# Kernel tuning notes

Hardware: AMD Instinct MI355X
Metric: run time of the kernel (lower is better)

The kernel has to match this reference:

```python
import jax, jax.numpy as jnp
import numpy as np

B, OUT, IN = 1024, 1024, 512


def setup_inputs() -> dict:
    key = jax.random.key(0)
    kx, kw = jax.random.split(key)
    X = jax.random.normal(kx, (B, IN), dtype=jnp.float32)
    # Xavier-uniform init for W [out_features, in_features]
    limit = float(np.sqrt(6.0 / (IN + OUT)))
    W = jax.random.uniform(kw, (OUT, IN), dtype=jnp.float32, minval=-limit, maxval=limit)
    return {"X": X, "W": W}


def reference(X, W):
    # tropical min-plus + max-plus 'matmul':
    # out[b,o] = min_i(W[o,i] + X[b,i]) + max_i(W[o,i] + X[b,i])
    S = X[:, None, :] + W[None, :, :]  # [B, OUT, IN]
    return jnp.min(S, axis=-1) + jnp.max(S, axis=-1)  # [B, OUT]
```

## Files before the change

### kernel.cpp

```cpp
#include <hip/hip_runtime.h>
#include <math.h>


typedef float f4 __attribute__((ext_vector_type(4)));

constexpr int B_DIM  = 1024;
constexpr int O_DIM  = 1024;
constexpr int IN_DIM = 512;

constexpr int TM     = 64;
constexpr int TN     = 32;
constexpr int KW     = 128;
constexpr int BK     = 8;
constexpr int NSTAGE = KW / BK;

__global__ __launch_bounds__(256) void tropical_gemm(
    const float* __restrict__ X, const float* __restrict__ W,
    float* __restrict__ out) {
    __shared__ float lds[8192];

    const int tid  = threadIdx.x;
    const int w    = tid >> 6;
    const int lane = tid & 63;
    const int im   = lane >> 3;
    const int in_  = lane & 7;
    const int b0   = blockIdx.y * TM;
    const int o0   = blockIdx.x * TN;
    const int xoff = im * 8;
    const int woff = in_ * 4;
    const int wrow = lane >> 1;
    const int wk4  = (lane & 1) * 4;

    const float* Xp = X + (size_t)(b0 + lane) * IN_DIM + w * KW;
    const float* Wp = W + (size_t)(o0 + wrow) * IN_DIM + w * KW + wk4;

    float* wbase = &lds[w * 1536];

    float mn[8][4], mx[8][4];
#pragma unroll
    for (int i = 0; i < 8; ++i)
#pragma unroll
        for (int j = 0; j < 4; ++j) { mn[i][j] = INFINITY; mx[i][j] = -INFINITY; }

#define STAGE(bufsel)                                                         \
    do {                                                                      \
        float* d_ = wbase + (bufsel) * 768;                                   \
        _Pragma("unroll")                                                     \
        for (int j_ = 0; j_ < 4; ++j_) {                                      \
            d_[j_ * 64 + lane]       = xa[j_];                                \
            d_[(4 + j_) * 64 + lane] = xb[j_];                                \
            d_[512 + (wk4 + j_) * 32 + wrow] = wv[j_];                        \
        }                                                                     \
    } while (0)

#define LOADQ(P, kp)                                                          \
    do {                                                                      \
        P##x0  = *(const f4*)(sXf + (2 * (kp)) * 64 + xoff);                  \
        P##x0b = *(const f4*)(sXf + (2 * (kp)) * 64 + xoff + 4);              \
        P##x1  = *(const f4*)(sXf + (2 * (kp) + 1) * 64 + xoff);              \
        P##x1b = *(const f4*)(sXf + (2 * (kp) + 1) * 64 + xoff + 4);          \
        P##w0  = *(const f4*)(sWf + (2 * (kp)) * 32 + woff);                  \
        P##w1  = *(const f4*)(sWf + (2 * (kp) + 1) * 32 + woff);              \
    } while (0)

#define COMPUTE(P)                                                            \
    do {                                                                      \
        _Pragma("unroll")                                                     \
        for (int a_ = 0; a_ < 8; ++a_) {                                      \
            const float x0_ = (a_ < 4) ? P##x0[a_] : P##x0b[a_ - 4];          \
            const float x1_ = (a_ < 4) ? P##x1[a_] : P##x1b[a_ - 4];          \
            _Pragma("unroll")                                                 \
            for (int b_ = 0; b_ < 4; ++b_) {                                  \
                float s0_ = x0_ + P##w0[b_];                                  \
                float s1_ = x1_ + P##w1[b_];                                  \
                asm("v_min3_f32 %0, %1, %2, %0"                               \
                    : "+v"(mn[a_][b_]) : "v"(s0_), "v"(s1_));                 \
                asm("v_max3_f32 %0, %1, %2, %0"                               \
                    : "+v"(mx[a_][b_]) : "v"(s0_), "v"(s1_));                 \
            }                                                                 \
        }                                                                     \
    } while (0)

    f4 xa = *(const f4*)(Xp);
    f4 xb = *(const f4*)(Xp + 4);
    f4 wv = *(const f4*)(Wp);
    STAGE(0);

#pragma unroll 1
    for (int s = 0; s < NSTAGE; ++s) {
        if (s + 1 < NSTAGE) {
            xa = *(const f4*)(Xp + (s + 1) * BK);
            xb = *(const f4*)(Xp + (s + 1) * BK + 4);
            wv = *(const f4*)(Wp + (s + 1) * BK);
        }

        const float* sXf = wbase + (s & 1) * 768;
        const float* sWf = sXf + 512;

        f4 Ax0, Ax0b, Ax1, Ax1b, Aw0, Aw1;
        f4 Bx0, Bx0b, Bx1, Bx1b, Bw0, Bw1;

        LOADQ(A, 0);
        LOADQ(B, 1);
        COMPUTE(A);
        LOADQ(A, 2);
        COMPUTE(B);
        LOADQ(B, 3);
        COMPUTE(A);
        COMPUTE(B);

        if (s + 1 < NSTAGE) STAGE((s + 1) & 1);
    }
#undef STAGE
#undef LOADQ
#undef COMPUTE

#define DUMP_STATE(slotbase)                                                  \
    do {                                                                      \
        float* p_ = (slotbase) + lane * 4;                                    \
        _Pragma("unroll")                                                     \
        for (int r_ = 0; r_ < 8; ++r_) {                                      \
            *(float4*)(p_ + r_ * 256) =                                       \
                make_float4(mn[r_][0], mn[r_][1], mn[r_][2], mn[r_][3]);      \
            *(float4*)(p_ + (8 + r_) * 256) =                                 \
                make_float4(mx[r_][0], mx[r_][1], mx[r_][2], mx[r_][3]);      \
        }                                                                     \
    } while (0)

#define MERGE_STATE(slotbase)                                                 \
    do {                                                                      \
        const float* p_ = (slotbase) + lane * 4;                              \
        _Pragma("unroll")                                                     \
        for (int r_ = 0; r_ < 8; ++r_) {                                      \
            float4 vn_ = *(const float4*)(p_ + r_ * 256);                     \
            float4 vx_ = *(const float4*)(p_ + (8 + r_) * 256);               \
            mn[r_][0] = fminf(mn[r_][0], vn_.x);                              \
            mn[r_][1] = fminf(mn[r_][1], vn_.y);                              \
            mn[r_][2] = fminf(mn[r_][2], vn_.z);                              \
            mn[r_][3] = fminf(mn[r_][3], vn_.w);                              \
            mx[r_][0] = fmaxf(mx[r_][0], vx_.x);                              \
            mx[r_][1] = fmaxf(mx[r_][1], vx_.y);                              \
            mx[r_][2] = fmaxf(mx[r_][2], vx_.z);                              \
            mx[r_][3] = fmaxf(mx[r_][3], vx_.w);                              \
        }                                                                     \
    } while (0)

    float* slotA = lds;
    float* slotB = lds + 4096;

    __syncthreads();
    if (w == 2) DUMP_STATE(slotA);
    if (w == 3) DUMP_STATE(slotB);
    __syncthreads();
    if (w == 0) MERGE_STATE(slotA);
    if (w == 1) MERGE_STATE(slotB);
    __syncthreads();
    if (w == 1) DUMP_STATE(slotA);
    __syncthreads();
    if (w == 0) {
        MERGE_STATE(slotA);
        float* op = out + (size_t)(b0 + im * 8) * O_DIM + o0 + in_ * 4;
#pragma unroll
        for (int r = 0; r < 8; ++r)
            *(float4*)(op + (size_t)r * O_DIM) =
                make_float4(mn[r][0] + mx[r][0], mn[r][1] + mx[r][1],
                            mn[r][2] + mx[r][2], mn[r][3] + mx[r][3]);
    }
#undef DUMP_STATE
#undef MERGE_STATE
}

extern "C" void kernel_launch(void* const* d_in, const int* in_sizes, int n_in,
                              void* d_out, int out_size, void* d_ws, size_t ws_size,
                              hipStream_t stream) {
    (void)in_sizes; (void)n_in; (void)d_ws; (void)ws_size; (void)out_size;
    const float* X = (const float*)d_in[0];
    const float* W = (const float*)d_in[1];
    float* out     = (float*)d_out;

    dim3 grid(O_DIM / TN, B_DIM / TM);
    tropical_gemm<<<grid, dim3(256), 0, stream>>>(X, W, out);
}
```

Before: 31.66 us.

## Use packed fp16 min/max accumulation for tropical GEMM inner loop

Converts X and W tiles to fp16 when staging into LDS and performs the add/min/max with packed half2 operations, processing two k-values per instruction, then reduces the two halves to fp32 at the end. It also deepens the prefetch by one stage and moves the next-stage LDS store earlier in the loop. This halves LDS traffic and per-element ALU instruction count but loses precision (fp16 sums of ~unit-scale values), which may exceed the correctness tolerance.

```diff
diff --git a/kernel.cpp b/kernel.cpp
--- a/kernel.cpp
+++ b/kernel.cpp
@@ -3,6 +3,9 @@
 
 
 typedef float f4 __attribute__((ext_vector_type(4)));
+typedef _Float16 h2 __attribute__((ext_vector_type(2)));
+
+struct __attribute__((aligned(16))) h2x4 { h2 h[4]; };
 
 constexpr int B_DIM  = 1024;
 constexpr int O_DIM  = 1024;
@@ -26,94 +29,109 @@
     const int in_  = lane & 7;
     const int b0   = blockIdx.y * TM;
     const int o0   = blockIdx.x * TN;
-    const int xoff = im * 8;
-    const int woff = in_ * 4;
     const int wrow = lane >> 1;
-    const int wk4  = (lane & 1) * 4;
+    const int wsel = lane & 1;
 
     const float* Xp = X + (size_t)(b0 + lane) * IN_DIM + w * KW;
-    const float* Wp = W + (size_t)(o0 + wrow) * IN_DIM + w * KW + wk4;
-
-    float* wbase = &lds[w * 1536];
-
-    float mn[8][4], mx[8][4];
-#pragma unroll
-    for (int i = 0; i < 8; ++i)
-#pragma unroll
-        for (int j = 0; j < 4; ++j) { mn[i][j] = INFINITY; mx[i][j] = -INFINITY; }
-
-#define STAGE(bufsel)                                                         \
-    do {                                                                      \
-        float* d_ = wbase + (bufsel) * 768;                                   \
-        _Pragma("unroll")                                                     \
-        for (int j_ = 0; j_ < 4; ++j_) {                                      \
-            d_[j_ * 64 + lane]       = xa[j_];                                \
-            d_[(4 + j_) * 64 + lane] = xb[j_];                                \
-            d_[512 + (wk4 + j_) * 32 + wrow] = wv[j_];                        \
-        }                                                                     \
-    } while (0)
-
-#define LOADQ(P, kp)                                                          \
-    do {                                                                      \
-        P##x0  = *(const f4*)(sXf + (2 * (kp)) * 64 + xoff);                  \
-        P##x0b = *(const f4*)(sXf + (2 * (kp)) * 64 + xoff + 4);              \
-        P##x1  = *(const f4*)(sXf + (2 * (kp) + 1) * 64 + xoff);              \
-        P##x1b = *(const f4*)(sXf + (2 * (kp) + 1) * 64 + xoff + 4);          \
-        P##w0  = *(const f4*)(sWf + (2 * (kp)) * 32 + woff);                  \
-        P##w1  = *(const f4*)(sWf + (2 * (kp) + 1) * 32 + woff);              \
+    const float* Wp = W + (size_t)(o0 + wrow) * IN_DIM + w * KW + wsel * 4;
+
+    char* wbase = (char*)lds + w * 3072;
+
+    h2 mn2[8][4], mx2[8][4];
+    {
+        const h2 pinf = {(_Float16)INFINITY, (_Float16)INFINITY};
+        const h2 ninf = {(_Float16)(-INFINITY), (_Float16)(-INFINITY)};
+#pragma unroll
+        for (int i = 0; i < 8; ++i)
+#pragma unroll
+            for (int j = 0; j < 4; ++j) { mn2[i][j] = pinf; mx2[i][j] = ninf; }
+    }
+
+#define PF(S)                                                                 \
+    do {                                                                      \
+        xa = *(const f4*)(Xp + (S) * BK);                                     \
+        xb = *(const f4*)(Xp + (S) * BK + 4);                                 \
+        wv = *(const f4*)(Wp + (S) * BK);                                     \
+    } while (0)
+
+#define STAGE(BUF)                                                            \
+    do {                                                                      \
+        char* dX_ = wbase + (BUF) * 1536;                                     \
+        char* dW_ = dX_ + 1024;                                               \
+        h2 p0_ = {(_Float16)xa[0], (_Float16)xa[1]};                          \
+        h2 p1_ = {(_Float16)xa[2], (_Float16)xa[3]};                          \
+        h2 p2_ = {(_Float16)xb[0], (_Float16)xb[1]};                          \
+        h2 p3_ = {(_Float16)xb[2], (_Float16)xb[3]};                          \
+        h2 q0_ = {(_Float16)wv[0], (_Float16)wv[1]};                          \
+        h2 q1_ = {(_Float16)wv[2], (_Float16)wv[3]};                          \
+        *(h2*)(dX_ + 0 * 256 + lane * 4) = p0_;                               \
+        *(h2*)(dX_ + 1 * 256 + lane * 4) = p1_;                               \
+        *(h2*)(dX_ + 2 * 256 + lane * 4) = p2_;                               \
+        *(h2*)(dX_ + 3 * 256 + lane * 4) = p3_;                               \
+        *(h2*)(dW_ + (wsel * 2 + 0) * 128 + wrow * 4) = q0_;                  \
+        *(h2*)(dW_ + (wsel * 2 + 1) * 128 + wrow * 4) = q1_;                  \
+    } while (0)
+
+#define LOADQ(P, SX, SW, KP)                                                  \
+    do {                                                                      \
+        P##xl = *(const h2x4*)((SX) + (KP) * 256 + im * 32);                  \
+        P##xh = *(const h2x4*)((SX) + (KP) * 256 + im * 32 + 16);             \
+        P##wq = *(const h2x4*)((SW) + (KP) * 128 + in_ * 16);                 \
     } while (0)
 
 #define COMPUTE(P)                                                            \
     do {                                                                      \
         _Pragma("unroll")                                                     \
         for (int a_ = 0; a_ < 8; ++a_) {                                      \
-            const float x0_ = (a_ < 4) ? P##x0[a_] : P##x0b[a_ - 4];          \
-            const float x1_ = (a_ < 4) ? P##x1[a_] : P##x1b[a_ - 4];          \
+            h2 xv_ = (a_ < 4) ? P##xl.h[a_ & 3] : P##xh.h[a_ & 3];            \
             _Pragma("unroll")                                                 \
             for (int b_ = 0; b_ < 4; ++b_) {                                  \
-                float s0_ = x0_ + P##w0[b_];                                  \
-                float s1_ = x1_ + P##w1[b_];                                  \
-                asm("v_min3_f32 %0, %1, %2, %0"                               \
-                    : "+v"(mn[a_][b_]) : "v"(s0_), "v"(s1_));                 \
-                asm("v_max3_f32 %0, %1, %2, %0"                               \
-                    : "+v"(mx[a_][b_]) : "v"(s0_), "v"(s1_));                 \
+                h2 s_ = xv_ + P##wq.h[b_];                                    \
+                mn2[a_][b_] = __builtin_elementwise_min(mn2[a_][b_], s_);     \
+                mx2[a_][b_] = __builtin_elementwise_max(mx2[a_][b_], s_);     \
             }                                                                 \
         }                                                                     \
     } while (0)
 
-    f4 xa = *(const f4*)(Xp);
-    f4 xb = *(const f4*)(Xp + 4);
-    f4 wv = *(const f4*)(Wp);
+    f4 xa, xb, wv;
+    PF(0);
     STAGE(0);
+    PF(1);
+
+    h2x4 Axl, Axh, Awq;
+    h2x4 Bxl, Bxh, Bwq;
 
 #pragma unroll 1
     for (int s = 0; s < NSTAGE; ++s) {
+        const char* sX = wbase + (s & 1) * 1536;
+        const char* sW = sX + 1024;
+
+        LOADQ(A, sX, sW, 0);
+        LOADQ(B, sX, sW, 1);
+        COMPUTE(A);
+        LOADQ(A, sX, sW, 2);
+        COMPUTE(B);
+        LOADQ(B, sX, sW, 3);
+        COMPUTE(A);
         if (s + 1 < NSTAGE) {
-            xa = *(const f4*)(Xp + (s + 1) * BK);
-            xb = *(const f4*)(Xp + (s + 1) * BK + 4);
-            wv = *(const f4*)(Wp + (s + 1) * BK);
+            STAGE((s + 1) & 1);
+            if (s + 2 < NSTAGE) PF(s + 2);
         }
-
-        const float* sXf = wbase + (s & 1) * 768;
-        const float* sWf = sXf + 512;
-
-        f4 Ax0, Ax0b, Ax1, Ax1b, Aw0, Aw1;
-        f4 Bx0, Bx0b, Bx1, Bx1b, Bw0, Bw1;
-
-        LOADQ(A, 0);
-        LOADQ(B, 1);
-        COMPUTE(A);
-        LOADQ(A, 2);
         COMPUTE(B);
-        LOADQ(B, 3);
-        COMPUTE(A);
-        COMPUTE(B);
-
-        if (s + 1 < NSTAGE) STAGE((s + 1) & 1);
     }
+#undef PF
 #undef STAGE
 #undef LOADQ
 #undef COMPUTE
+
+    float mn[8][4], mx[8][4];
+#pragma unroll
+    for (int r = 0; r < 8; ++r)
+#pragma unroll
+        for (int c = 0; c < 4; ++c) {
+            mn[r][c] = fminf((float)mn2[r][c][0], (float)mn2[r][c][1]);
+            mx[r][c] = fmaxf((float)mx2[r][c][0], (float)mx2[r][c][1]);
+        }
 
 #define DUMP_STATE(slotbase)                                                  \
     do {                                                                      \
```

New measurement: 38.30 us. +20.9%, slower.
